# Kernel tuning notes

Hardware: AMD Instinct MI355X
Metric: run time of the kernel (lower is better)

## Reference

```python
import jax, jax.numpy as jnp
import numpy as np

N_NODES = 100000
N_EDGES = 3200000


def gcn_conv(x, src, dst, ew, W, b, num_nodes):
    """PyG GCNConv: h = x@W; out[dst] += norm * h[src]; norm = d^-1/2[src]*w*d^-1/2[dst].
    src/dst/ew must already include self-loops (weight 1)."""
    h = x @ W  # [N, F_out]
    deg = jax.ops.segment_sum(ew, dst, num_segments=num_nodes)  # weighted in-degree
    dinv = jnp.where(deg > 0, jax.lax.rsqrt(deg), 0.0)
    norm = dinv[src] * ew * dinv[dst]  # [E]
    msg = h[src] * norm[:, None]  # [E, F_out] gather + scale
    out = jax.ops.segment_sum(msg, dst, num_segments=num_nodes)  # scatter-add
    return out + b


def setup_inputs() -> dict:
    key = jax.random.key(0)
    k1, k2, k3, k4, k5 = jax.random.split(key, 5)
    x = jax.random.normal(k1, (N_NODES, 35), dtype=jnp.float32)
    edge_index = jax.random.randint(k2, (2, N_EDGES), 0, N_NODES, dtype=jnp.int64)
    edge_weight = jax.random.uniform(k3, (N_EDGES,), dtype=jnp.float32)
    W1 = jax.random.normal(k4, (35, 64), dtype=jnp.float32) * (1.0 / np.sqrt(35))
    b1 = jnp.zeros((64,), dtype=jnp.float32)
    W2 = jax.random.normal(k5, (64, 2), dtype=jnp.float32) * (1.0 / np.sqrt(64))
    b2 = jnp.zeros((2,), dtype=jnp.float32)
    return {"x": x, "edge_index": edge_index, "edge_weight": edge_weight,
            "W1": W1, "b1": b1, "W2": W2, "b2": b2}


def reference(x, edge_index, edge_weight, W1, b1, W2, b2):
    n = x.shape[0]
    # add self-loops with weight 1 (PyG default fill_value=1), static shapes
    loop = jnp.arange(n, dtype=edge_index.dtype)
    src = jnp.concatenate([edge_index[0], loop])
    dst = jnp.concatenate([edge_index[1], loop])
    ew = jnp.concatenate([edge_weight, jnp.ones((n,), dtype=edge_weight.dtype)])

    h = jax.nn.relu(gcn_conv(x, src, dst, ew, W1, b1, n))
    h = gcn_conv(h, src, dst, ew, W2, b2, n)
    return jax.nn.log_softmax(h, axis=1)
```

## Files before the change

### kernel.cpp

```cpp
#include <hip/hip_runtime.h>
#include <hip/hip_fp16.h>
#include <math.h>

#define FIN 35
#define F1  64
#define BSZ 256
#define BSH 8
#define GSH 7
#define MAXNB 512
#define PCH 8192
#define SCAP 12288

__global__ void k_hist(const int* __restrict__ dst, int* __restrict__ cmat,
                       int E, int NB, int NCHUNK) {
    __shared__ int h[MAXNB];
    int c = blockIdx.x, t = threadIdx.x;
    for (int i = t; i < NB; i += 256) h[i] = 0;
    __syncthreads();
    int e0 = c * PCH, e1 = min(e0 + PCH, E);
    bool al = ((size_t)(dst + e0) & 15) == 0;
    int nv = al ? ((e1 - e0) >> 2) : 0;
    const int4* d4 = (const int4*)(dst + e0);
    for (int i = t; i < nv; i += 256) {
        int4 v = d4[i];
        atomicAdd(&h[v.x >> BSH], 1); atomicAdd(&h[v.y >> BSH], 1);
        atomicAdd(&h[v.z >> BSH], 1); atomicAdd(&h[v.w >> BSH], 1);
    }
    for (int e = e0 + (nv << 2) + t; e < e1; e += 256) atomicAdd(&h[dst[e] >> BSH], 1);
    __syncthreads();
    for (int i = t; i < NB; i += 256) cmat[(size_t)i * NCHUNK + c] = h[i];
}

__global__ void k_scan_row(int* __restrict__ cmat, int* __restrict__ rsum, int NCHUNK) {
    __shared__ int s[512];
    int b = blockIdx.x, t = threadIdx.x;
    int v = (t < NCHUNK) ? cmat[(size_t)b * NCHUNK + t] : 0;
    s[t] = v;
    __syncthreads();
    #pragma unroll
    for (int off = 1; off < 512; off <<= 1) {
        int tv = (t >= off) ? s[t - off] : 0;
        __syncthreads();
        s[t] += tv;
        __syncthreads();
    }
    if (t < NCHUNK) cmat[(size_t)b * NCHUNK + t] = s[t] - v;
    if (t == 511) rsum[b] = s[511];
}

__global__ void k_scan_buck(const int* __restrict__ rsum, int* __restrict__ bbase,
                            int* __restrict__ boff, int NB, int E) {
    __shared__ int s[1024];
    int t = threadIdx.x;
    int v = (t < NB) ? rsum[t] : 0;
    s[t] = v;
    __syncthreads();
    #pragma unroll
    for (int off = 1; off < 1024; off <<= 1) {
        int tv = (t >= off) ? s[t - off] : 0;
        __syncthreads();
        s[t] += tv;
        __syncthreads();
    }
    if (t < NB) {
        int excl = s[t] - v;
        bbase[t] = excl;
        boff[t] = excl;
    }
    if (t == 0) boff[NB] = E;
}

__global__ __launch_bounds__(512) void k_place(
        const int* __restrict__ src, const int* __restrict__ dst,
        const float* __restrict__ ew, const int* __restrict__ cmat,
        const int* __restrict__ bbase,
        int2* __restrict__ recs, int E, int NB, int NCHUNK) {
    extern __shared__ char pmem[];
    int2* lrec   = (int2*)pmem;
    int*  addr32 = (int*)(lrec + PCH);
    __shared__ int s[512];
    __shared__ int lbase[512];
    __shared__ int cur[512];
    __shared__ int gwin[512];
    int c = blockIdx.x, t = threadIdx.x;
    s[t] = 0;
    __syncthreads();
    int e0 = c * PCH, e1 = min(e0 + PCH, E);
    bool al = (((size_t)(dst + e0) | (size_t)(src + e0) | (size_t)(ew + e0)) & 15) == 0;
    int nv = al ? ((e1 - e0) >> 2) : 0;
    const int4*   s4 = (const int4*)(src + e0);
    const int4*   d4 = (const int4*)(dst + e0);
    const float4* w4 = (const float4*)(ew + e0);
    for (int i = t; i < nv; i += 512) {
        int4 v = d4[i];
        atomicAdd(&s[v.x >> BSH], 1); atomicAdd(&s[v.y >> BSH], 1);
        atomicAdd(&s[v.z >> BSH], 1); atomicAdd(&s[v.w >> BSH], 1);
    }
    for (int e = e0 + (nv << 2) + t; e < e1; e += 512) atomicAdd(&s[dst[e] >> BSH], 1);
    __syncthreads();
    int v = s[t];
    __syncthreads();
    #pragma unroll
    for (int off = 1; off < 512; off <<= 1) {
        int tv = (t >= off) ? s[t - off] : 0;
        __syncthreads();
        s[t] += tv;
        __syncthreads();
    }
    lbase[t] = s[t] - v;
    cur[t] = 0;
    gwin[t] = (t < NB) ? (cmat[(size_t)t * NCHUNK + c] + bbase[t]) : 0;
    __syncthreads();
    for (int i = t; i < nv; i += 512) {
        int4   sv = s4[i];
        int4   dv = d4[i];
        float4 wv = w4[i];
        int b, r, sl;
        b = dv.x >> BSH; r = atomicAdd(&cur[b], 1); sl = lbase[b] + r;
        lrec[sl] = make_int2(sv.x | ((dv.x & (BSZ-1)) << 24), __float_as_int(wv.x));
        addr32[sl] = gwin[b] + r;
        b = dv.y >> BSH; r = atomicAdd(&cur[b], 1); sl = lbase[b] + r;
        lrec[sl] = make_int2(sv.y | ((dv.y & (BSZ-1)) << 24), __float_as_int(wv.y));
        addr32[sl] = gwin[b] + r;
        b = dv.z >> BSH; r = atomicAdd(&cur[b], 1); sl = lbase[b] + r;
        lrec[sl] = make_int2(sv.z | ((dv.z & (BSZ-1)) << 24), __float_as_int(wv.z));
        addr32[sl] = gwin[b] + r;
        b = dv.w >> BSH; r = atomicAdd(&cur[b], 1); sl = lbase[b] + r;
        lrec[sl] = make_int2(sv.w | ((dv.w & (BSZ-1)) << 24), __float_as_int(wv.w));
        addr32[sl] = gwin[b] + r;
    }
    for (int e = e0 + (nv << 2) + t; e < e1; e += 512) {
        int d = dst[e];
        int b = d >> BSH;
        int r = atomicAdd(&cur[b], 1);
        int sl = lbase[b] + r;
        lrec[sl] = make_int2(src[e] | ((d & (BSZ-1)) << 24), __float_as_int(ew[e]));
        addr32[sl] = gwin[b] + r;
    }
    __syncthreads();
    int cnt = e1 - e0;
    for (int i = t; i < cnt; i += 512) recs[addr32[i]] = lrec[i];
}

__global__ __launch_bounds__(1024) void k_sort(
        const int* __restrict__ boff, const int2* __restrict__ recs_in,
        int2* __restrict__ recs_out, int* __restrict__ row_ptr,
        float* __restrict__ dinv, int n) {
    extern __shared__ unsigned short inv16[];
    __shared__ int   hcnt[BSZ];
    __shared__ int   hoff[BSZ];
    __shared__ float dsum[BSZ];
    int b = blockIdx.x, t = threadIdx.x;
    if (t < BSZ) { hcnt[t] = 0; dsum[t] = 1.0f; }
    __syncthreads();
    int s0 = boff[b], s1 = boff[b + 1];
    int cnt = s1 - s0;
    for (int i = t; i < cnt; i += 1024) {
        int2 rc = recs_in[s0 + i];
        int dl = ((unsigned)rc.x) >> 24;
        atomicAdd(&hcnt[dl], 1);
        atomicAdd(&dsum[dl], __int_as_float(rc.y));
    }
    __syncthreads();
    int v = 0;
    if (t < BSZ) { v = hcnt[t]; hoff[t] = v; }
    __syncthreads();
    #pragma unroll
    for (int off = 1; off < BSZ; off <<= 1) {
        int tv = 0;
        if (t < BSZ && t >= off) tv = hoff[t - off];
        __syncthreads();
        if (t < BSZ) hoff[t] += tv;
        __syncthreads();
    }
    if (t < BSZ) {
        int excl = hoff[t] - v;
        int node = b * BSZ + t;
        if (node < n) {
            row_ptr[node] = s0 + excl;
            dinv[node] = rsqrtf(dsum[t]);
            if (node == n - 1) row_ptr[n] = s1;
        }
        hcnt[t] = excl;
    }
    __syncthreads();
    if (cnt <= SCAP) {
        for (int i = t; i < cnt; i += 1024) {
            int2 rc = recs_in[s0 + i];
            int dl = ((unsigned)rc.x) >> 24;
            int pos = atomicAdd(&hcnt[dl], 1);
            inv16[pos] = (unsigned short)i;
        }
        __syncthreads();
        for (int o = t; o < cnt; o += 1024) {
            int2 rc = recs_in[s0 + inv16[o]];
            recs_out[s0 + o] = make_int2((rc.x & 0xFFFFFF) << GSH, rc.y);
        }
    } else {
        for (int i = t; i < cnt; i += 1024) {
            int2 rc = recs_in[s0 + i];
            int dl = ((unsigned)rc.x) >> 24;
            int pos = atomicAdd(&hcnt[dl], 1);
            recs_out[s0 + pos] = make_int2((rc.x & 0xFFFFFF) << GSH, rc.y);
        }
    }
}

__global__ void k_gemm1(const float* __restrict__ x, const float* __restrict__ W1,
                        const float* __restrict__ dinv, __half* __restrict__ g1, int n) {
    __shared__ float W1s[FIN * F1];
    __shared__ float xs[64 * FIN];
    int t = threadIdx.x;
    for (int i = t; i < FIN * F1; i += 256) W1s[i] = W1[i];
    int row0 = blockIdx.x * 64;
    int nrows = min(64, n - row0);
    for (int i = t; i < nrows * FIN; i += 256) xs[i] = x[(size_t)row0 * FIN + i];
    __syncthreads();
    int wave = t >> 6, f = t & 63;
    for (int rl = wave; rl < nrows; rl += 4) {
        float acc = 0.0f;
        #pragma unroll
        for (int k = 0; k < FIN; k++) acc += xs[rl * FIN + k] * W1s[k * F1 + f];
        int row = row0 + rl;
        g1[(size_t)row * F1 + f] = __float2half(acc * dinv[row]);
    }
}

__global__ void k_gather1(const int* __restrict__ rp, const int2* __restrict__ csr,
                          const __half* __restrict__ g1,
                          const float* __restrict__ dinv, const float* __restrict__ b1,
                          const float* __restrict__ W2, float* __restrict__ g2, int n) {
    int wid = (int)((blockIdx.x * (long long)blockDim.x + threadIdx.x) >> 6);
    int f = threadIdx.x & 63;
    if (wid >= n) return;
    const char* g1b = (const char*)g1 + f * 2;
    int start = rp[wid], end = rp[wid + 1];
    float acc = 0.0f;
    int e = start;
    for (; e + 16 <= end; e += 16) {
        float a[16];
        int2 r[16];
        #pragma unroll
        for (int j = 0; j < 16; j++) r[j] = csr[e + j];
        #pragma unroll
        for (int j = 0; j < 16; j++)
            a[j] = __half2float(*(const __half*)(g1b + (unsigned)r[j].x));
        #pragma unroll
        for (int j = 0; j < 16; j++) acc += __int_as_float(r[j].y) * a[j];
    }
    for (; e + 4 <= end; e += 4) {
        int2 r0 = csr[e], r1 = csr[e+1], r2 = csr[e+2], r3 = csr[e+3];
        float a0 = __half2float(*(const __half*)(g1b + (unsigned)r0.x));
        float a1 = __half2float(*(const __half*)(g1b + (unsigned)r1.x));
        float a2 = __half2float(*(const __half*)(g1b + (unsigned)r2.x));
        float a3 = __half2float(*(const __half*)(g1b + (unsigned)r3.x));
        acc += __int_as_float(r0.y) * a0; acc += __int_as_float(r1.y) * a1;
        acc += __int_as_float(r2.y) * a2; acc += __int_as_float(r3.y) * a3;
    }
    for (; e < end; e++) {
        int2 r = csr[e];
        acc += __int_as_float(r.y) * __half2float(*(const __half*)(g1b + (unsigned)r.x));
    }
    float dv = dinv[wid];
    float h = dv * (acc + __half2float(g1[(size_t)wid * F1 + f])) + b1[f];
    h = h > 0.0f ? h : 0.0f;
    float2 w2v = ((const float2*)W2)[f];
    float z0 = h * w2v.x, z1 = h * w2v.y;
    #pragma unroll
    for (int off = 32; off > 0; off >>= 1) {
        z0 += __shfl_xor(z0, off, 64);
        z1 += __shfl_xor(z1, off, 64);
    }
    if (f == 0) {
        g2[(size_t)wid * 2 + 0] = dv * z0;
        g2[(size_t)wid * 2 + 1] = dv * z1;
    }
}

__global__ void k_gather2(const int* __restrict__ rp, const int2* __restrict__ csr,
                          const float* __restrict__ g2,
                          const float* __restrict__ dinv, const float* __restrict__ b2,
                          float* __restrict__ out, int n) {
    int wid = (int)((blockIdx.x * (long long)blockDim.x + threadIdx.x) >> 6);
    int lane = threadIdx.x & 63;
    if (wid >= n) return;
    const char* g2b = (const char*)g2;
    int start = rp[wid], end = rp[wid + 1];
    float a0 = 0.0f, a1 = 0.0f;
    int e = start + lane;
    for (; e + 192 < end; e += 256) {
        int2 q0 = csr[e], q1 = csr[e + 64], q2 = csr[e + 128], q3 = csr[e + 192];
        float2 v0 = *(const float2*)(g2b + (((unsigned)q0.x) >> 4));
        float2 v1 = *(const float2*)(g2b + (((unsigned)q1.x) >> 4));
        float2 v2 = *(const float2*)(g2b + (((unsigned)q2.x) >> 4));
        float2 v3 = *(const float2*)(g2b + (((unsigned)q3.x) >> 4));
        a0 += __int_as_float(q0.y) * v0.x; a1 += __int_as_float(q0.y) * v0.y;
        a0 += __int_as_float(q1.y) * v1.x; a1 += __int_as_float(q1.y) * v1.y;
        a0 += __int_as_float(q2.y) * v2.x; a1 += __int_as_float(q2.y) * v2.y;
        a0 += __int_as_float(q3.y) * v3.x; a1 += __int_as_float(q3.y) * v3.y;
    }
    for (; e < end; e += 64) {
        int2 r = csr[e];
        float w = __int_as_float(r.y);
        float2 gv = *(const float2*)(g2b + (((unsigned)r.x) >> 4));
        a0 += w * gv.x; a1 += w * gv.y;
    }
    #pragma unroll
    for (int off = 32; off > 0; off >>= 1) {
        a0 += __shfl_xor(a0, off, 64);
        a1 += __shfl_xor(a1, off, 64);
    }
    if (lane == 0) {
        float dv = dinv[wid];
        float2 sv = ((const float2*)g2)[wid];
        float z0 = dv * (a0 + sv.x) + b2[0];
        float z1 = dv * (a1 + sv.y) + b2[1];
        float m = fmaxf(z0, z1);
        float lse = m + logf(expf(z0 - m) + expf(z1 - m));
        ((float2*)out)[wid] = make_float2(z0 - lse, z1 - lse);
    }
}

extern "C" void kernel_launch(void* const* d_in, const int* in_sizes, int n_in,
                              void* d_out, int out_size, void* d_ws, size_t ws_size,
                              hipStream_t stream) {
    const float* x  = (const float*)d_in[0];
    const int*   ei = (const int*)d_in[1];
    const float* ew = (const float*)d_in[2];
    const float* W1 = (const float*)d_in[3];
    const float* b1 = (const float*)d_in[4];
    const float* W2 = (const float*)d_in[5];
    const float* b2 = (const float*)d_in[6];
    float* out = (float*)d_out;

    int n = in_sizes[0] / FIN;
    int E = in_sizes[2];
    const int* src = ei;
    const int* dst = ei + E;
    int NB = (n + BSZ - 1) / BSZ;
    int NCHUNK = (E + PCH - 1) / PCH;
    int M = NB * NCHUNK;

    char* ws = (char*)d_ws;
    size_t off = 0;
    auto alloc = [&](size_t bytes) -> void* {
        void* p = ws + off;
        off += (bytes + 15) & ~(size_t)15;
        return p;
    };
    int*    cmat    = (int*)   alloc((size_t)M * 4);
    int*    rsum    = (int*)   alloc((size_t)NB * 4);
    int*    bbase   = (int*)   alloc((size_t)NB * 4);
    int*    boff    = (int*)   alloc((size_t)(NB + 1) * 4);
    int*    row_ptr = (int*)   alloc((size_t)(n + 1) * 4);
    float*  dinv    = (float*) alloc((size_t)n * 4);
    int2*   recs_a  = (int2*)  alloc((size_t)E * 8);
    int2*   recs_b  = (int2*)  alloc((size_t)E * 8);
    __half* g1      = (__half*)alloc((size_t)n * F1 * 2);
    float*  g2      = (float*) alloc((size_t)n * 2 * 4);

    size_t place_lds = (size_t)PCH * 8 + (size_t)PCH * 4;
    size_t sort_lds  = (size_t)SCAP * 2;

    k_hist     <<<NCHUNK, 256, 0, stream>>>(dst, cmat, E, NB, NCHUNK);
    k_scan_row <<<NB, 512, 0, stream>>>(cmat, rsum, NCHUNK);
    k_scan_buck<<<1, 1024, 0, stream>>>(rsum, bbase, boff, NB, E);
    k_place    <<<NCHUNK, 512, place_lds, stream>>>(src, dst, ew, cmat, bbase, recs_a, E, NB, NCHUNK);
    k_sort     <<<NB, 1024, sort_lds, stream>>>(boff, recs_a, recs_b, row_ptr, dinv, n);
    k_gemm1    <<<(n + 63) / 64, 256, 0, stream>>>(x, W1, dinv, g1, n);
    k_gather1  <<<(n + 3) / 4, 256, 0, stream>>>(row_ptr, recs_b, g1, dinv, b1, W2, g2, n);
    k_gather2  <<<(n + 3) / 4, 256, 0, stream>>>(row_ptr, recs_b, g2, dinv, b2, out, n);
}
```

Baseline: 305.7 us.

## Halve sort block size, vectorize gemm1 loads, use half-wave per node in gather2

The sort kernel now runs with 512 threads per block instead of 1024, which lets more blocks be resident at once. The gemm1 shared-memory staging of W1 and x switches to float4 loads with a scalar tail. gather2 now assigns 32 lanes to each node, so one wave covers two nodes, which suits the roughly 33 edges per node and cuts idle lanes and shuffle steps. The float4 load of x assumes that row0*35 floats is 16-byte aligned, which holds because row0 is a multiple of 64.

```diff
diff --git a/kernel.cpp b/kernel.cpp
--- a/kernel.cpp
+++ b/kernel.cpp
@@ -142,7 +142,7 @@
     for (int i = t; i < cnt; i += 512) recs[addr32[i]] = lrec[i];
 }
 
-__global__ __launch_bounds__(1024) void k_sort(
+__global__ __launch_bounds__(512) void k_sort(
         const int* __restrict__ boff, const int2* __restrict__ recs_in,
         int2* __restrict__ recs_out, int* __restrict__ row_ptr,
         float* __restrict__ dinv, int n) {
@@ -155,7 +155,7 @@
     __syncthreads();
     int s0 = boff[b], s1 = boff[b + 1];
     int cnt = s1 - s0;
-    for (int i = t; i < cnt; i += 1024) {
+    for (int i = t; i < cnt; i += 512) {
         int2 rc = recs_in[s0 + i];
         int dl = ((unsigned)rc.x) >> 24;
         atomicAdd(&hcnt[dl], 1);
@@ -185,19 +185,19 @@
     }
     __syncthreads();
     if (cnt <= SCAP) {
-        for (int i = t; i < cnt; i += 1024) {
+        for (int i = t; i < cnt; i += 512) {
             int2 rc = recs_in[s0 + i];
             int dl = ((unsigned)rc.x) >> 24;
             int pos = atomicAdd(&hcnt[dl], 1);
             inv16[pos] = (unsigned short)i;
         }
         __syncthreads();
-        for (int o = t; o < cnt; o += 1024) {
+        for (int o = t; o < cnt; o += 512) {
             int2 rc = recs_in[s0 + inv16[o]];
             recs_out[s0 + o] = make_int2((rc.x & 0xFFFFFF) << GSH, rc.y);
         }
     } else {
-        for (int i = t; i < cnt; i += 1024) {
+        for (int i = t; i < cnt; i += 512) {
             int2 rc = recs_in[s0 + i];
             int dl = ((unsigned)rc.x) >> 24;
             int pos = atomicAdd(&hcnt[dl], 1);
@@ -211,10 +211,14 @@
     __shared__ float W1s[FIN * F1];
     __shared__ float xs[64 * FIN];
     int t = threadIdx.x;
-    for (int i = t; i < FIN * F1; i += 256) W1s[i] = W1[i];
+    for (int i = t; i < (FIN * F1) / 4; i += 256) ((float4*)W1s)[i] = ((const float4*)W1)[i];
     int row0 = blockIdx.x * 64;
     int nrows = min(64, n - row0);
-    for (int i = t; i < nrows * FIN; i += 256) xs[i] = x[(size_t)row0 * FIN + i];
+    const float* xbase = x + (size_t)row0 * FIN;
+    int tot = nrows * FIN;
+    int totv = tot >> 2;
+    for (int i = t; i < totv; i += 256) ((float4*)xs)[i] = ((const float4*)xbase)[i];
+    for (int i = (totv << 2) + t; i < tot; i += 256) xs[i] = xbase[i];
     __syncthreads();
     int wave = t >> 6, f = t & 63;
     for (int rl = wave; rl < nrows; rl += 4) {
@@ -281,15 +285,17 @@
                           const float* __restrict__ g2,
                           const float* __restrict__ dinv, const float* __restrict__ b2,
                           float* __restrict__ out, int n) {
-    int wid = (int)((blockIdx.x * (long long)blockDim.x + threadIdx.x) >> 6);
+    int w = (int)((blockIdx.x * (long long)blockDim.x + threadIdx.x) >> 6);
     int lane = threadIdx.x & 63;
-    if (wid >= n) return;
+    int half = lane >> 5, sub = lane & 31;
+    int node = w * 2 + half;
+    if (node >= n) return;
     const char* g2b = (const char*)g2;
-    int start = rp[wid], end = rp[wid + 1];
+    int start = rp[node], end = rp[node + 1];
     float a0 = 0.0f, a1 = 0.0f;
-    int e = start + lane;
-    for (; e + 192 < end; e += 256) {
-        int2 q0 = csr[e], q1 = csr[e + 64], q2 = csr[e + 128], q3 = csr[e + 192];
+    int e = start + sub;
+    for (; e + 96 < end; e += 128) {
+        int2 q0 = csr[e], q1 = csr[e + 32], q2 = csr[e + 64], q3 = csr[e + 96];
         float2 v0 = *(const float2*)(g2b + (((unsigned)q0.x) >> 4));
         float2 v1 = *(const float2*)(g2b + (((unsigned)q1.x) >> 4));
         float2 v2 = *(const float2*)(g2b + (((unsigned)q2.x) >> 4));
@@ -299,25 +305,25 @@
         a0 += __int_as_float(q2.y) * v2.x; a1 += __int_as_float(q2.y) * v2.y;
         a0 += __int_as_float(q3.y) * v3.x; a1 += __int_as_float(q3.y) * v3.y;
     }
-    for (; e < end; e += 64) {
+    for (; e < end; e += 32) {
         int2 r = csr[e];
-        float w = __int_as_float(r.y);
+        float wt = __int_as_float(r.y);
         float2 gv = *(const float2*)(g2b + (((unsigned)r.x) >> 4));
-        a0 += w * gv.x; a1 += w * gv.y;
-    }
-    #pragma unroll
-    for (int off = 32; off > 0; off >>= 1) {
+        a0 += wt * gv.x; a1 += wt * gv.y;
+    }
+    #pragma unroll
+    for (int off = 16; off > 0; off >>= 1) {
         a0 += __shfl_xor(a0, off, 64);
         a1 += __shfl_xor(a1, off, 64);
     }
-    if (lane == 0) {
-        float dv = dinv[wid];
-        float2 sv = ((const float2*)g2)[wid];
+    if (sub == 0) {
+        float dv = dinv[node];
+        float2 sv = ((const float2*)g2)[node];
         float z0 = dv * (a0 + sv.x) + b2[0];
         float z1 = dv * (a1 + sv.y) + b2[1];
         float m = fmaxf(z0, z1);
         float lse = m + logf(expf(z0 - m) + expf(z1 - m));
-        ((float2*)out)[wid] = make_float2(z0 - lse, z1 - lse);
+        ((float2*)out)[node] = make_float2(z0 - lse, z1 - lse);
     }
 }
 
@@ -362,12 +368,14 @@
     size_t place_lds = (size_t)PCH * 8 + (size_t)PCH * 4;
     size_t sort_lds  = (size_t)SCAP * 2;
 
+    int g2_waves = (n + 1) / 2 + 1;
+
     k_hist     <<<NCHUNK, 256, 0, stream>>>(dst, cmat, E, NB, NCHUNK);
     k_scan_row <<<NB, 512, 0, stream>>>(cmat, rsum, NCHUNK);
     k_scan_buck<<<1, 1024, 0, stream>>>(rsum, bbase, boff, NB, E);
     k_place    <<<NCHUNK, 512, place_lds, stream>>>(src, dst, ew, cmat, bbase, recs_a, E, NB, NCHUNK);
-    k_sort     <<<NB, 1024, sort_lds, stream>>>(boff, recs_a, recs_b, row_ptr, dinv, n);
+    k_sort     <<<NB, 512, sort_lds, stream>>>(boff, recs_a, recs_b, row_ptr, dinv, n);
     k_gemm1    <<<(n + 63) / 64, 256, 0, stream>>>(x, W1, dinv, g1, n);
     k_gather1  <<<(n + 3) / 4, 256, 0, stream>>>(row_ptr, recs_b, g1, dinv, b1, W2, g2, n);
-    k_gather2  <<<(n + 3) / 4, 256, 0, stream>>>(row_ptr, recs_b, g2, dinv, b2, out, n);
-}
+    k_gather2  <<<(g2_waves + 3) / 4, 256, 0, stream>>>(row_ptr, recs_b, g2, dinv, b2, out, n);
+}
```

Result: faster. 297.3 us (-2.7%).
